# Optimization experiments

Measured on AMD Instinct MI355X. Metric: run time of the kernel, lower is better.

## Reference

```python
import jax, jax.numpy as jnp
import numpy as np

B, S, E, H = 4, 2048, 1024, 16
D = E // H  # head_dim = 64

def setup_inputs() -> dict:
    key = jax.random.key(0)
    ks = jax.random.split(key, 9)
    std = 1.0 / np.sqrt(E)
    return {
        "x":  jax.random.normal(ks[0], (B, S, E), jnp.float32),
        "Wq": jax.random.uniform(ks[1], (E, E), jnp.float32, -std, std),
        "bq": jax.random.uniform(ks[2], (E,),   jnp.float32, -std, std),
        "Wk": jax.random.uniform(ks[3], (E, E), jnp.float32, -std, std),
        "bk": jax.random.uniform(ks[4], (E,),   jnp.float32, -std, std),
        "Wv": jax.random.uniform(ks[5], (E, E), jnp.float32, -std, std),
        "bv": jax.random.uniform(ks[6], (E,),   jnp.float32, -std, std),
        "Wo": jax.random.uniform(ks[7], (E, E), jnp.float32, -std, std),
        "bo": jax.random.uniform(ks[8], (E,),   jnp.float32, -std, std),
    }

def reference(x, Wq, bq, Wk, bk, Wv, bv, Wo, bo):
    b, s, e = x.shape
    # QKV projections (weights stored as [in,out] == torch W.T applied as x @ W)
    q = (x @ Wq + bq).reshape(b, s, H, D).transpose(0, 2, 1, 3)  # [B,H,S,D]
    k = (x @ Wk + bk).reshape(b, s, H, D).transpose(0, 2, 1, 3)
    v = (x @ Wv + bv).reshape(b, s, H, D).transpose(0, 2, 1, 3)
    scores = jnp.einsum('bhqd,bhkd->bhqk', q, k) / jnp.sqrt(jnp.float32(D))
    causal = jnp.triu(jnp.ones((s, s), bool), k=1)  # True above diagonal
    scores = jnp.where(causal, -jnp.inf, scores)
    p = jax.nn.softmax(scores, axis=-1)  # dropout disabled (eval mode)
    out = jnp.einsum('bhqk,bhkd->bhqd', p, v)  # [B,H,S,D]
    out = out.transpose(0, 2, 1, 3).reshape(b, s, e)
    return out @ Wo + bo
```

## Files before the change

### kernel.cpp

```cpp
#include <hip/hip_runtime.h>
#include <math.h>

#define E_DIM 1024
#define B_DIM 4
#define S_DIM 2048
#define H_DIM 16
#define D_HEAD 64
#define M_DIM (B_DIM * S_DIM)
#define LOG2E 1.44269504f
#define RESCALE_THR 4.0f

typedef _Float16 half8 __attribute__((ext_vector_type(8)));
typedef _Float16 half4 __attribute__((ext_vector_type(4)));
typedef __fp16  fp16x2 __attribute__((ext_vector_type(2)));
typedef float floatx4 __attribute__((ext_vector_type(4)));
#define MFMA_F16(a, b, c) __builtin_amdgcn_mfma_f32_16x16x32_f16(a, b, c, 0, 0, 0)

#if __has_builtin(__builtin_amdgcn_exp2f)
#define EXP2F(x) __builtin_amdgcn_exp2f(x)
#else
#define EXP2F(x) exp2f(x)
#endif

union H4 { fp16x2 h2[2]; half4 h4; };

#define GLDS16(g, l)                                                          \
    __builtin_amdgcn_global_load_lds(                                         \
        (const __attribute__((address_space(1))) void*)(g),                   \
        (__attribute__((address_space(3))) void*)(l), 16, 0, 0)

__device__ const int SEG_QBLK[40] = {3,4,5,6,7,7,8,8,9,9,10,10,11,11,11,12,12,12,
                                     13,13,13,14,14,14,15,15,15,15,
                                     2,6,10,14, 1,5,9,13, 0,4,8,12};
__device__ const int SEG_SEG[40]  = {0,0,0,0,0,1,0,1,0,1,0,1,0,1,2,0,1,2,
                                     0,1,2,0,1,2,0,1,2,3,
                                     0,1,2,3, 0,1,2,3, 0,1,2,3};
__device__ const int SEG_BASE[16] = {0,1,2,3,4,6,8,10,12,15,18,21,24,28,32,36};

__global__ __launch_bounds__(256) void cvt_x(
    const float* __restrict__ X, _Float16* __restrict__ Xh)
{
    size_t i = ((size_t)blockIdx.x * 256 + threadIdx.x) * 8;
    float4 a = *(const float4*)&X[i];
    float4 b = *(const float4*)&X[i + 4];
    half8 h = {(_Float16)a.x, (_Float16)a.y, (_Float16)a.z, (_Float16)a.w,
               (_Float16)b.x, (_Float16)b.y, (_Float16)b.z, (_Float16)b.w};
    *(half8*)&Xh[i] = h;
}

__global__ __launch_bounds__(256) void cvt_w(
    const float* __restrict__ W0, const float* __restrict__ W1,
    const float* __restrict__ W2, const float* __restrict__ W3,
    _Float16* __restrict__ T0, _Float16* __restrict__ T1,
    _Float16* __restrict__ T2, _Float16* __restrict__ T3)
{
    const int z = blockIdx.z;
    const float* W = (z == 0) ? W0 : (z == 1) ? W1 : (z == 2) ? W2 : W3;
    _Float16*   T  = (z == 0) ? T0 : (z == 1) ? T1 : (z == 2) ? T2 : T3;
    const int k0 = blockIdx.x * 64, n0 = blockIdx.y * 64;
    const int tid = threadIdx.x;
    __shared__ float t[64][65];
#pragma unroll
    for (int it = 0; it < 4; it++) {
        int r = it * 16 + (tid >> 4);
        int c = (tid & 15) * 4;
        float4 v = *(const float4*)&W[(size_t)(k0 + r) * E_DIM + n0 + c];
        t[r][c] = v.x; t[r][c + 1] = v.y; t[r][c + 2] = v.z; t[r][c + 3] = v.w;
    }
    __syncthreads();
#pragma unroll
    for (int it = 0; it < 2; it++) {
        int n = it * 32 + (tid >> 3);
        int kk = (tid & 7) * 8;
        half8 h;
#pragma unroll
        for (int j = 0; j < 8; j++) h[j] = (_Float16)t[kk + j][n];
        *(half8*)&T[(size_t)(n0 + n) * E_DIM + k0 + kk] = h;
    }
}

#define GEMM_CORE(Aptr, Bptr)                                                 \
    const int tid = threadIdx.x;                                              \
    const int wave = tid >> 6, lane = tid & 63;                               \
    const int m16 = lane & 15, quad = lane >> 4;                              \
    const int wm = (wave >> 1) * 64, wn = (wave & 1) * 64;                    \
    const int m0 = blockIdx.x * 128, n0 = blockIdx.y * 128;                   \
    __shared__ _Float16 As[128 * 32];                                         \
    __shared__ _Float16 Bs[128 * 32];                                         \
    floatx4 acc[4][4];                                                        \
    const floatx4 zf = {0.f, 0.f, 0.f, 0.f};                                  \
    _Pragma("unroll") for (int i = 0; i < 4; i++)                             \
        _Pragma("unroll") for (int j = 0; j < 4; j++) acc[i][j] = zf;         \
    const int lrow = lane >> 2, lseg = lane & 3;                              \
    const _Float16* gA = (Aptr) + (size_t)(m0 + wave * 32 + lrow) * E_DIM + lseg * 8; \
    const _Float16* gB = (Bptr) + (size_t)(n0 + wave * 32 + lrow) * E_DIM + lseg * 8; \
    _Float16* lA = As + (wave * 32) * 32;                                     \
    _Float16* lB = Bs + (wave * 32) * 32;                                     \
    for (int k0 = 0; k0 < E_DIM; k0 += 32) {                                  \
        __syncthreads();                                                      \
        GLDS16(gA + k0, lA);                                                  \
        GLDS16(gA + 16 * E_DIM + k0, lA + 16 * 32);                           \
        GLDS16(gB + k0, lB);                                                  \
        GLDS16(gB + 16 * E_DIM + k0, lB + 16 * 32);                           \
        __syncthreads();                                                      \
        half8 af[4], bf[4];                                                   \
        _Pragma("unroll") for (int mt = 0; mt < 4; mt++)                      \
            af[mt] = *(const half8*)&As[(wm + mt * 16 + m16) * 32 + quad * 8];\
        _Pragma("unroll") for (int nt = 0; nt < 4; nt++)                      \
            bf[nt] = *(const half8*)&Bs[(wn + nt * 16 + m16) * 32 + quad * 8];\
        _Pragma("unroll") for (int mt = 0; mt < 4; mt++)                      \
            _Pragma("unroll") for (int nt = 0; nt < 4; nt++)                  \
                acc[mt][nt] = MFMA_F16(af[mt], bf[nt], acc[mt][nt]);          \
    }

__global__ __launch_bounds__(256) void qkv_mfma(
    const _Float16* __restrict__ Xh,
    const _Float16* __restrict__ Tq, const float* __restrict__ bq,
    const _Float16* __restrict__ Tk, const float* __restrict__ bk,
    const _Float16* __restrict__ Tv, const float* __restrict__ bv,
    _Float16* __restrict__ Qo, _Float16* __restrict__ Ko, _Float16* __restrict__ Vo)
{
    const int z = blockIdx.z;
    const _Float16* Wt   = (z == 0) ? Tq : (z == 1) ? Tk : Tv;
    const float*    bias = (z == 0) ? bq : (z == 1) ? bk : bv;

    GEMM_CORE(Xh, Wt)

    if (z == 2) {
#pragma unroll
        for (int nt = 0; nt < 4; nt++) {
            int n = n0 + wn + nt * 16 + m16;
            int h = n >> 6, d = n & 63;
            int dt = d >> 4, ld = d & 15;
            float bias_v = bias[n];
#pragma unroll
            for (int mt = 0; mt < 4; mt++) {
                int m_b = m0 + wm + mt * 16 + quad * 4;
                int b = m_b >> 11, s = m_b & 2047;
                int bh = b * H_DIM + h;
                int c = s >> 6, kl = s & 63;
                int kh = kl >> 5, q8 = (kl >> 3) & 3, j0 = kl & 7;
                size_t off = ((size_t)bh * 32 + c) * 4096
                           + (size_t)(((dt * 2 + kh) * 64 + q8 * 16 + ld) * 8 + j0);
                half4 hv;
#pragma unroll
                for (int r = 0; r < 4; r++) hv[r] = (_Float16)(acc[mt][nt][r] + bias_v);
                *(half4*)&Vo[off] = hv;
            }
        }
    } else {
        _Float16* Out = (z == 0) ? Qo : Ko;
        const float sc = (z == 0) ? 0.125f * LOG2E : 1.0f;
#pragma unroll
        for (int nt = 0; nt < 4; nt++) {
            int n = n0 + wn + nt * 16 + m16;
            int h = n >> 6, d = n & 63;
            int dh = d >> 5, qd = (d >> 3) & 3, j = d & 7;
            float bias_v = bias[n];
#pragma unroll
            for (int mt = 0; mt < 4; mt++) {
#pragma unroll
                for (int r = 0; r < 4; r++) {
                    int m = m0 + wm + mt * 16 + quad * 4 + r;
                    int b = m >> 11, s = m & 2047;
                    int bh = b * H_DIM + h;
                    size_t off;
                    if (z == 0) {
                        int qblk = s >> 7, qq = s & 127;
                        int sub = qq >> 4, lq = qq & 15;
                        off = ((size_t)bh * 16 + qblk) * 8192
                            + (size_t)(((sub * 2 + dh) * 64 + qd * 16 + lq) * 8 + j);
                    } else {
                        int c = s >> 6, kl = s & 63;
                        int kt = kl >> 4, lk = kl & 15;
                        off = ((size_t)bh * 32 + c) * 4096
                            + (size_t)(((kt * 2 + dh) * 64 + qd * 16 + lk) * 8 + j);
                    }
                    Out[off] = (_Float16)((acc[mt][nt][r] + bias_v) * sc);
                }
            }
        }
    }
}

__global__ __launch_bounds__(256) void out_mfma(
    const _Float16* __restrict__ Oh, const _Float16* __restrict__ To,
    const float* __restrict__ bias, float* __restrict__ Out)
{
    GEMM_CORE(Oh, To)

#pragma unroll
    for (int nt = 0; nt < 4; nt++) {
        int n = n0 + wn + nt * 16 + m16;
        float bias_v = bias[n];
#pragma unroll
        for (int mt = 0; mt < 4; mt++) {
#pragma unroll
            for (int r = 0; r < 4; r++) {
                int m = m0 + wm + mt * 16 + quad * 4 + r;
                Out[(size_t)m * E_DIM + n] = acc[mt][nt][r] + bias_v;
            }
        }
    }
}

__global__ __launch_bounds__(256) void attn_mfma(
    const _Float16* __restrict__ Qb, const _Float16* __restrict__ Kb,
    const _Float16* __restrict__ Vb, _Float16* __restrict__ Opart,
    float* __restrict__ Mv, float* __restrict__ Lv, _Float16* __restrict__ O)
{
    const int bh = blockIdx.y;
    const int wid = blockIdx.x;
    const int qblk = SEG_QBLK[wid];
    const int seg  = SEG_SEG[wid];
    const int q0 = qblk * 128;
    const int c0 = seg * 8;
    const int c1 = min(c0 + 8, 2 * qblk + 2);
    const bool solo = (c0 == 0) && (c1 == 2 * qblk + 2);
    const int tid = threadIdx.x;
    const int wave = tid >> 6, lane = tid & 63;
    const int m16 = lane & 15, quad = lane >> 4;
    const int sw = m16 & 7;

    __shared__ _Float16 Ps[8192];
    _Float16* Pw = Ps + wave * 2048;

    const int qmin = q0 + wave * 32;
    const int qmax = qmin + 31;
    const int c1w = min(c1, (qmax >> 6) + 1);

    const _Float16* gQ = Qb + ((size_t)bh * 16 + qblk) * 8192 + wave * 2048 + lane * 8;
    half8 qf[2][2];
#pragma unroll
    for (int mt = 0; mt < 2; mt++)
#pragma unroll
        for (int dh = 0; dh < 2; dh++)
            qf[mt][dh] = *(const half8*)&gQ[(mt * 2 + dh) * 512];

    _Float16* pwp[2][4];
    const _Float16* pfp[2][2];
#pragma unroll
    for (int mt = 0; mt < 2; mt++) {
#pragma unroll
        for (int kt = 0; kt < 4; kt++) {
            int kb = kt * 2 + (quad >> 1);
            pwp[mt][kt] = &Pw[(mt * 16 + m16) * 64 + ((kb ^ sw) << 3) + ((quad & 1) << 2)];
        }
#pragma unroll
        for (int kh = 0; kh < 2; kh++)
            pfp[mt][kh] = &Pw[(mt * 16 + m16) * 64 + (((kh * 4 + quad) ^ sw) << 3)];
    }

    float m_i[2] = {-INFINITY, -INFINITY}, l_i[2] = {0.f, 0.f};
    floatx4 acco[2][4];
    const floatx4 zf = {0.f, 0.f, 0.f, 0.f};
#pragma unroll
    for (int mt = 0; mt < 2; mt++)
#pragma unroll
        for (int dt = 0; dt < 4; dt++) acco[mt][dt] = zf;

    const _Float16* gK = Kb + ((size_t)bh * 32 + c0) * 4096 + lane * 8;
    const _Float16* gV = Vb + ((size_t)bh * 32 + c0) * 4096 + lane * 8;

    half8 kf[4][2];
#pragma unroll
    for (int kt = 0; kt < 4; kt++)
#pragma unroll
        for (int dh = 0; dh < 2; dh++)
            kf[kt][dh] = *(const half8*)&gK[(kt * 2 + dh) * 512];
    gK += 4096;

    for (int c = c0; c < c1w; c++) {
        const int k0 = c * 64;

        half8 vf[4][2];
#pragma unroll
        for (int dt = 0; dt < 4; dt++)
#pragma unroll
            for (int kh = 0; kh < 2; kh++)
                vf[dt][kh] = *(const half8*)&gV[(dt * 2 + kh) * 512];
        gV += 4096;

        floatx4 sf[2][4];
        __builtin_amdgcn_s_setprio(1);
#pragma unroll
        for (int kt = 0; kt < 4; kt++)
#pragma unroll
            for (int mt = 0; mt < 2; mt++)
                sf[mt][kt] = MFMA_F16(kf[kt][1], qf[mt][1],
                               MFMA_F16(kf[kt][0], qf[mt][0], zf));
        __builtin_amdgcn_s_setprio(0);

        if (c + 1 < c1w) {
#pragma unroll
            for (int kt = 0; kt < 4; kt++)
#pragma unroll
                for (int dh = 0; dh < 2; dh++)
                    kf[kt][dh] = *(const half8*)&gK[(kt * 2 + dh) * 512];
            gK += 4096;
        }

        const bool full = (k0 + 63 <= qmin);
#pragma unroll
        for (int mt = 0; mt < 2; mt++) {
            const int qg = qmin + mt * 16 + m16;
            float mx = -INFINITY;
#pragma unroll
            for (int kt = 0; kt < 4; kt++)
#pragma unroll
                for (int r = 0; r < 4; r++) {
                    float v = sf[mt][kt][r];
                    if (!full) {
                        int key = k0 + kt * 16 + quad * 4 + r;
                        v = (key <= qg) ? v : -INFINITY;
                    }
                    sf[mt][kt][r] = v;
                    mx = fmaxf(mx, v);
                }
            mx = fmaxf(mx, __shfl_xor(mx, 16));
            mx = fmaxf(mx, __shfl_xor(mx, 32));
            float mn = m_i[mt];
            if (!__all(mx <= mn + RESCALE_THR)) {
                mn = fmaxf(mn, mx);
                float alpha = EXP2F(m_i[mt] - mn);
                m_i[mt] = mn;
                l_i[mt] *= alpha;
#pragma unroll
                for (int dt = 0; dt < 4; dt++) acco[mt][dt] *= alpha;
            }
            float ls = 0.f;
#pragma unroll
            for (int kt = 0; kt < 4; kt++) {
                float e0 = EXP2F(sf[mt][kt][0] - mn);
                float e1 = EXP2F(sf[mt][kt][1] - mn);
                float e2 = EXP2F(sf[mt][kt][2] - mn);
                float e3 = EXP2F(sf[mt][kt][3] - mn);
                ls += (e0 + e1) + (e2 + e3);
                H4 u;
                u.h2[0] = __builtin_amdgcn_cvt_pkrtz(e0, e1);
                u.h2[1] = __builtin_amdgcn_cvt_pkrtz(e2, e3);
                *(half4*)pwp[mt][kt] = u.h4;
            }
            ls += __shfl_xor(ls, 16);
            ls += __shfl_xor(ls, 32);
            l_i[mt] += ls;
        }
        asm volatile("s_waitcnt lgkmcnt(0)" ::: "memory");

        half8 pf[2][2];
#pragma unroll
        for (int mt = 0; mt < 2; mt++)
#pragma unroll
            for (int kh = 0; kh < 2; kh++)
                pf[mt][kh] = *(const half8*)pfp[mt][kh];
        __builtin_amdgcn_s_setprio(1);
#pragma unroll
        for (int dt = 0; dt < 4; dt++)
#pragma unroll
            for (int mt = 0; mt < 2; mt++)
                acco[mt][dt] = MFMA_F16(vf[dt][1], pf[mt][1],
                                 MFMA_F16(vf[dt][0], pf[mt][0], acco[mt][dt]));
        __builtin_amdgcn_s_setprio(0);
    }

    if (solo) {
        const int b = bh >> 4;
        const int h = bh & (H_DIM - 1);
#pragma unroll
        for (int mt = 0; mt < 2; mt++) {
            float inv = 1.f / l_i[mt];
            int q = qmin + mt * 16 + m16;
            _Float16* dst = O + (size_t)(b * S_DIM + q) * E_DIM + h * 64;
#pragma unroll
            for (int dt = 0; dt < 4; dt++) {
                H4 u;
                u.h2[0] = __builtin_amdgcn_cvt_pkrtz(acco[mt][dt][0] * inv, acco[mt][dt][1] * inv);
                u.h2[1] = __builtin_amdgcn_cvt_pkrtz(acco[mt][dt][2] * inv, acco[mt][dt][3] * inv);
                *(half4*)&dst[dt * 16 + quad * 4] = u.h4;
            }
        }
    } else {
        const size_t prow = ((size_t)bh * 40 + SEG_BASE[qblk] + seg) * 128;
#pragma unroll
        for (int mt = 0; mt < 2; mt++) {
            int lq = wave * 32 + mt * 16 + m16;
            if (quad == 0) {
                Mv[prow + lq] = m_i[mt];
                Lv[prow + lq] = l_i[mt];
            }
            _Float16* dst = Opart + (prow + lq) * 64;
#pragma unroll
            for (int dt = 0; dt < 4; dt++) {
                H4 u;
                u.h2[0] = __builtin_amdgcn_cvt_pkrtz(acco[mt][dt][0], acco[mt][dt][1]);
                u.h2[1] = __builtin_amdgcn_cvt_pkrtz(acco[mt][dt][2], acco[mt][dt][3]);
                *(half4*)&dst[dt * 16 + quad * 4] = u.h4;
            }
        }
    }
}

__global__ __launch_bounds__(256) void attn_combine(
    const _Float16* __restrict__ Opart, const float* __restrict__ Mv,
    const float* __restrict__ Lv, _Float16* __restrict__ O)
{
    const int qb = blockIdx.x + 4, bh = blockIdx.y;
    const int nseg = (qb >> 2) + 1;
    const size_t pbase = ((size_t)bh * 40 + SEG_BASE[qb]) * 128;
    const int t = threadIdx.x;
    const int r = t >> 1, dh = (t & 1) * 32;

    float m_s[4], w[4];
    float M = -INFINITY;
    for (int s = 0; s < nseg; s++) {
        m_s[s] = Mv[pbase + s * 128 + r];
        M = fmaxf(M, m_s[s]);
    }
    float L = 0.f;
    for (int s = 0; s < nseg; s++) {
        w[s] = EXP2F(m_s[s] - M);
        L += Lv[pbase + s * 128 + r] * w[s];
    }
    const float invL = 1.f / L;

    const int b = bh >> 4, h = bh & (H_DIM - 1);
    const int q = qb * 128 + r;
    _Float16* dst = O + (size_t)(b * S_DIM + q) * E_DIM + h * 64 + dh;
#pragma unroll
    for (int d0 = 0; d0 < 32; d0 += 8) {
        float acc[8] = {0.f, 0.f, 0.f, 0.f, 0.f, 0.f, 0.f, 0.f};
        for (int s = 0; s < nseg; s++) {
            half8 v = *(const half8*)&Opart[(pbase + s * 128 + r) * 64 + dh + d0];
#pragma unroll
            for (int j = 0; j < 8; j++) acc[j] += w[s] * (float)v[j];
        }
        half8 o;
#pragma unroll
        for (int j = 0; j < 8; j++) o[j] = (_Float16)(acc[j] * invL);
        *(half8*)&dst[d0] = o;
    }
}

extern "C" void kernel_launch(void* const* d_in, const int* in_sizes, int n_in,
                              void* d_out, int out_size, void* d_ws, size_t ws_size,
                              hipStream_t stream) {
    const float* x  = (const float*)d_in[0];
    const float* Wq = (const float*)d_in[1];
    const float* bq = (const float*)d_in[2];
    const float* Wk = (const float*)d_in[3];
    const float* bk = (const float*)d_in[4];
    const float* Wv = (const float*)d_in[5];
    const float* bv = (const float*)d_in[6];
    const float* Wo = (const float*)d_in[7];
    const float* bo = (const float*)d_in[8];

    const size_t SZ = (size_t)M_DIM * E_DIM;
    const size_t WZ = (size_t)E_DIM * E_DIM;
    _Float16* Xh = (_Float16*)d_ws;
    _Float16* Tq = Xh + SZ;
    _Float16* Tk = Tq + WZ;
    _Float16* Tv = Tk + WZ;
    _Float16* To = Tv + WZ;
    _Float16* Qb = To + WZ;
    _Float16* Kb = Qb + SZ;
    _Float16* Vb = Kb + SZ;
    _Float16* Opart = Vb + SZ;
    float* Mv = (float*)(Opart + (size_t)2560 * 8192);
    float* Lv = Mv + 2560 * 128;
    _Float16* Oh = Xh;

    cvt_x<<<dim3(M_DIM * E_DIM / 2048), 256, 0, stream>>>(x, Xh);
    cvt_w<<<dim3(16, 16, 4), 256, 0, stream>>>(Wq, Wk, Wv, Wo, Tq, Tk, Tv, To);

    qkv_mfma<<<dim3(M_DIM / 128, E_DIM / 128, 3), 256, 0, stream>>>(
        Xh, Tq, bq, Tk, bk, Tv, bv, Qb, Kb, Vb);

    attn_mfma<<<dim3(40, B_DIM * H_DIM), 256, 0, stream>>>(
        Qb, Kb, Vb, Opart, Mv, Lv, Oh);

    attn_combine<<<dim3(12, B_DIM * H_DIM), 256, 0, stream>>>(Opart, Mv, Lv, Oh);

    out_mfma<<<dim3(M_DIM / 128, E_DIM / 128), 256, 0, stream>>>(
        Oh, To, bo, (float*)d_out);
}
```

Baseline: 305.8 us.

## Keep softmax probabilities in registers by permuting V layout; split attention into single-wave blocks

Permutes the key ordering in the V output layout so the exp'd probability fragments from the QK MFMA can feed the PV MFMA directly as B operands. This removes the LDS round trip for P (stores, waitcnt, reloads) and the shared memory allocation. Attention blocks become one wave each (160x64 grid) since waves no longer share LDS. Cross-lane reductions use permlane16/32 swap where available instead of shuffles. The risk is a wrong layout permutation, and losing any benefit the four waves got from sharing K/V fetches within one block.

Result: no change. 311.4 us (+1.8%).

```diff
diff --git a/kernel.cpp b/kernel.cpp
--- a/kernel.cpp
+++ b/kernel.cpp
@@ -14,6 +14,7 @@
 typedef _Float16 half4 __attribute__((ext_vector_type(4)));
 typedef __fp16  fp16x2 __attribute__((ext_vector_type(2)));
 typedef float floatx4 __attribute__((ext_vector_type(4)));
+typedef unsigned uint2v __attribute__((ext_vector_type(2)));
 #define MFMA_F16(a, b, c) __builtin_amdgcn_mfma_f32_16x16x32_f16(a, b, c, 0, 0, 0)
 
 #if __has_builtin(__builtin_amdgcn_exp2f)
@@ -23,6 +24,26 @@
 #endif
 
 union H4 { fp16x2 h2[2]; half4 h4; };
+union H8 { fp16x2 h2[4]; half8 h8; };
+
+__device__ inline float red_xor16(float x, int lane) {
+#if __has_builtin(__builtin_amdgcn_permlane16_swap)
+    uint2v r = __builtin_amdgcn_permlane16_swap(
+        __builtin_bit_cast(unsigned, x), __builtin_bit_cast(unsigned, x), false, false);
+    return __builtin_bit_cast(float, (lane & 16) ? r[0] : r[1]);
+#else
+    return __shfl_xor(x, 16);
+#endif
+}
+__device__ inline float red_xor32(float x, int lane) {
+#if __has_builtin(__builtin_amdgcn_permlane32_swap)
+    uint2v r = __builtin_amdgcn_permlane32_swap(
+        __builtin_bit_cast(unsigned, x), __builtin_bit_cast(unsigned, x), false, false);
+    return __builtin_bit_cast(float, (lane & 32) ? r[0] : r[1]);
+#else
+    return __shfl_xor(x, 32);
+#endif
+}
 
 #define GLDS16(g, l)                                                          \
     __builtin_amdgcn_global_load_lds(                                         \
@@ -139,7 +160,7 @@
                 int b = m_b >> 11, s = m_b & 2047;
                 int bh = b * H_DIM + h;
                 int c = s >> 6, kl = s & 63;
-                int kh = kl >> 5, q8 = (kl >> 3) & 3, j0 = kl & 7;
+                int kh = kl >> 5, q8 = (kl >> 2) & 3, j0 = ((kl >> 4) & 1) * 4;
                 size_t off = ((size_t)bh * 32 + c) * 4096
                            + (size_t)(((dt * 2 + kh) * 64 + q8 * 16 + ld) * 8 + j0);
                 half4 hv;
@@ -204,26 +225,22 @@
     }
 }
 
-__global__ __launch_bounds__(256) void attn_mfma(
+__global__ __launch_bounds__(64) void attn_mfma(
     const _Float16* __restrict__ Qb, const _Float16* __restrict__ Kb,
     const _Float16* __restrict__ Vb, _Float16* __restrict__ Opart,
     float* __restrict__ Mv, float* __restrict__ Lv, _Float16* __restrict__ O)
 {
     const int bh = blockIdx.y;
-    const int wid = blockIdx.x;
+    const int wid = blockIdx.x >> 2;
+    const int wave = blockIdx.x & 3;
     const int qblk = SEG_QBLK[wid];
     const int seg  = SEG_SEG[wid];
     const int q0 = qblk * 128;
     const int c0 = seg * 8;
     const int c1 = min(c0 + 8, 2 * qblk + 2);
     const bool solo = (c0 == 0) && (c1 == 2 * qblk + 2);
-    const int tid = threadIdx.x;
-    const int wave = tid >> 6, lane = tid & 63;
+    const int lane = threadIdx.x;
     const int m16 = lane & 15, quad = lane >> 4;
-    const int sw = m16 & 7;
-
-    __shared__ _Float16 Ps[8192];
-    _Float16* Pw = Ps + wave * 2048;
 
     const int qmin = q0 + wave * 32;
     const int qmax = qmin + 31;
@@ -236,20 +253,6 @@
 #pragma unroll
         for (int dh = 0; dh < 2; dh++)
             qf[mt][dh] = *(const half8*)&gQ[(mt * 2 + dh) * 512];
-
-    _Float16* pwp[2][4];
-    const _Float16* pfp[2][2];
-#pragma unroll
-    for (int mt = 0; mt < 2; mt++) {
-#pragma unroll
-        for (int kt = 0; kt < 4; kt++) {
-            int kb = kt * 2 + (quad >> 1);
-            pwp[mt][kt] = &Pw[(mt * 16 + m16) * 64 + ((kb ^ sw) << 3) + ((quad & 1) << 2)];
-        }
-#pragma unroll
-        for (int kh = 0; kh < 2; kh++)
-            pfp[mt][kh] = &Pw[(mt * 16 + m16) * 64 + (((kh * 4 + quad) ^ sw) << 3)];
-    }
 
     float m_i[2] = {-INFINITY, -INFINITY}, l_i[2] = {0.f, 0.f};
     floatx4 acco[2][4];
@@ -304,21 +307,24 @@
 #pragma unroll
         for (int mt = 0; mt < 2; mt++) {
             const int qg = qmin + mt * 16 + m16;
-            float mx = -INFINITY;
 #pragma unroll
             for (int kt = 0; kt < 4; kt++)
 #pragma unroll
                 for (int r = 0; r < 4; r++) {
-                    float v = sf[mt][kt][r];
                     if (!full) {
                         int key = k0 + kt * 16 + quad * 4 + r;
-                        v = (key <= qg) ? v : -INFINITY;
+                        if (key > qg) sf[mt][kt][r] = -INFINITY;
                     }
-                    sf[mt][kt][r] = v;
-                    mx = fmaxf(mx, v);
                 }
-            mx = fmaxf(mx, __shfl_xor(mx, 16));
-            mx = fmaxf(mx, __shfl_xor(mx, 32));
+            float mk[4];
+#pragma unroll
+            for (int kt = 0; kt < 4; kt++)
+                mk[kt] = fmaxf(fmaxf(sf[mt][kt][0], sf[mt][kt][1]),
+                               fmaxf(sf[mt][kt][2], sf[mt][kt][3]));
+            float mx = fmaxf(fmaxf(mk[0], mk[1]), fmaxf(mk[2], mk[3]));
+            mx = fmaxf(mx, red_xor16(mx, lane));
+            mx = fmaxf(mx, red_xor32(mx, lane));
+
             float mn = m_i[mt];
             if (!__all(mx <= mn + RESCALE_THR)) {
                 mn = fmaxf(mn, mx);
@@ -328,7 +334,9 @@
 #pragma unroll
                 for (int dt = 0; dt < 4; dt++) acco[mt][dt] *= alpha;
             }
+
             float ls = 0.f;
+            H8 u[2];
 #pragma unroll
             for (int kt = 0; kt < 4; kt++) {
                 float e0 = EXP2F(sf[mt][kt][0] - mn);
@@ -336,31 +344,20 @@
                 float e2 = EXP2F(sf[mt][kt][2] - mn);
                 float e3 = EXP2F(sf[mt][kt][3] - mn);
                 ls += (e0 + e1) + (e2 + e3);
-                H4 u;
-                u.h2[0] = __builtin_amdgcn_cvt_pkrtz(e0, e1);
-                u.h2[1] = __builtin_amdgcn_cvt_pkrtz(e2, e3);
-                *(half4*)pwp[mt][kt] = u.h4;
-            }
-            ls += __shfl_xor(ls, 16);
-            ls += __shfl_xor(ls, 32);
+                u[kt >> 1].h2[(kt & 1) * 2]     = __builtin_amdgcn_cvt_pkrtz(e0, e1);
+                u[kt >> 1].h2[(kt & 1) * 2 + 1] = __builtin_amdgcn_cvt_pkrtz(e2, e3);
+            }
+            ls += red_xor16(ls, lane);
+            ls += red_xor32(ls, lane);
             l_i[mt] += ls;
-        }
-        asm volatile("s_waitcnt lgkmcnt(0)" ::: "memory");
-
-        half8 pf[2][2];
-#pragma unroll
-        for (int mt = 0; mt < 2; mt++)
-#pragma unroll
-            for (int kh = 0; kh < 2; kh++)
-                pf[mt][kh] = *(const half8*)pfp[mt][kh];
-        __builtin_amdgcn_s_setprio(1);
-#pragma unroll
-        for (int dt = 0; dt < 4; dt++)
-#pragma unroll
-            for (int mt = 0; mt < 2; mt++)
-                acco[mt][dt] = MFMA_F16(vf[dt][1], pf[mt][1],
-                                 MFMA_F16(vf[dt][0], pf[mt][0], acco[mt][dt]));
-        __builtin_amdgcn_s_setprio(0);
+
+            __builtin_amdgcn_s_setprio(1);
+#pragma unroll
+            for (int dt = 0; dt < 4; dt++)
+                acco[mt][dt] = MFMA_F16(vf[dt][1], u[1].h8,
+                                 MFMA_F16(vf[dt][0], u[0].h8, acco[mt][dt]));
+            __builtin_amdgcn_s_setprio(0);
+        }
     }
 
     if (solo) {
@@ -475,7 +472,7 @@
     qkv_mfma<<<dim3(M_DIM / 128, E_DIM / 128, 3), 256, 0, stream>>>(
         Xh, Tq, bq, Tk, bk, Tv, bv, Qb, Kb, Vb);
 
-    attn_mfma<<<dim3(40, B_DIM * H_DIM), 256, 0, stream>>>(
+    attn_mfma<<<dim3(160, B_DIM * H_DIM), 64, 0, stream>>>(
         Qb, Kb, Vb, Opart, Mv, Lv, Oh);
 
     attn_combine<<<dim3(12, B_DIM * H_DIM), 256, 0, stream>>>(Opart, Mv, Lv, Oh);
```
